# Kernel tuning notes

Measured on AMD Instinct MI355X. Metric: run time of the kernel, lower is better.

The kernel has to match this reference:

```python
import jax, jax.numpy as jnp
import numpy as np

N_NODES = 100000
N_EDGES = 1000000
LATENT = 128
EMBED = 32


def setup_inputs() -> dict:
    key = jax.random.key(0)
    ks = jax.random.split(key, 10)
    z = jax.random.normal(ks[0], (N_NODES, LATENT), dtype=jnp.float32)
    edge_index = jax.random.randint(ks[1], (2, N_EDGES), 0, N_NODES, dtype=jnp.int64)
    bond_types = jax.random.randint(ks[2], (N_EDGES,), 0, 13, dtype=jnp.int64)
    d_in = 2 * LATENT + EMBED  # 288
    s = lambda k, shape, fan: jax.random.normal(k, shape, dtype=jnp.float32) / np.sqrt(fan)
    embed = s(ks[3], (13, EMBED), EMBED)
    W1 = s(ks[4], (d_in, LATENT), d_in)
    b1 = jnp.zeros((LATENT,), jnp.float32)
    W2 = s(ks[5], (LATENT, 64), LATENT)
    b2 = jnp.zeros((64,), jnp.float32)
    W3 = s(ks[6], (64, 1), 64)
    b3 = jnp.zeros((1,), jnp.float32)
    return {"z": z, "edge_index": edge_index, "bond_types": bond_types,
            "embed": embed, "W1": W1, "b1": b1, "W2": W2, "b2": b2,
            "W3": W3, "b3": b3}


def reference(z, edge_index, bond_types, embed, W1, b1, W2, b2, W3, b3):
    src, dst = edge_index[0], edge_index[1]
    # gather endpoint latents and bond-type embedding, concat -> [E, 288]
    features = jnp.concatenate([z[src], z[dst], embed[bond_types]], axis=-1)
    h = jax.nn.relu(features @ W1 + b1)   # dropout is identity in eval mode
    h = jax.nn.relu(h @ W2 + b2)
    out = jax.nn.softplus(h @ W3 + b3)
    return out.squeeze(-1)  # [E]
```

## Files before the change

### kernel.cpp

```cpp
#include <hip/hip_runtime.h>

#define E_EDGES 1000000
#define BM 64
#define NBLK (E_EDGES / BM)
#define DIN 288
#define PADA 296
#define H1DIM 128
#define PAD1 136
#define H2DIM 64
#define PAD2 68
#define NNODES 100000
#define LATENT 128

#define WT1_OFF 0
#define WT2_OFF (DIN * H1DIM)
#define EMB_OFF (WT2_OFF + H1DIM * H2DIM)
#define ZB_OFF  46080
#define WS_NEED ((size_t)(ZB_OFF + NNODES * LATENT) * 2)

typedef __bf16 v8bf __attribute__((ext_vector_type(8)));
typedef __bf16 v4bf __attribute__((ext_vector_type(4)));
typedef float  v4f  __attribute__((ext_vector_type(4)));

__device__ __forceinline__ void cvt_store4(__bf16* p, float4 v) {
    v4bf o;
    o[0] = (__bf16)v.x; o[1] = (__bf16)v.y; o[2] = (__bf16)v.z; o[3] = (__bf16)v.w;
    *(v4bf*)p = o;
}

__global__ void prep_kernel(const float* __restrict__ W1, const float* __restrict__ W2,
                            const float* __restrict__ z, const float* __restrict__ embed,
                            __bf16* __restrict__ ws, int do_z) {
    int i = blockIdx.x * 256 + threadIdx.x;
    if (do_z) {
        int i4 = i * 4;
        if (i4 < NNODES * LATENT) {
            float4 v = *(const float4*)(z + i4);
            cvt_store4(ws + ZB_OFF + i4, v);
        }
    }
    if (i < DIN * H1DIM) {
        int n = i / DIN, k = i - n * DIN;
        ws[WT1_OFF + i] = (__bf16)W1[k * H1DIM + n];
    }
    if (i < H1DIM * H2DIM) {
        int n = i / H1DIM, k = i - n * H1DIM;
        ws[WT2_OFF + i] = (__bf16)W2[k * H2DIM + n];
    }
    if (i < 13 * 32) ws[EMB_OFF + i] = (__bf16)embed[i];
}

template <bool ZBF16>
__global__ __launch_bounds__(256, 4) void fused_kernel(
    const float* __restrict__ z, const int* __restrict__ eidx,
    const int* __restrict__ bt, const float* __restrict__ embed,
    const float* __restrict__ b1, const float* __restrict__ b2,
    const float* __restrict__ W3, const float* __restrict__ b3,
    const __bf16* __restrict__ ws, float* __restrict__ out)
{
    __shared__ __bf16 sA[BM * PADA];
    __shared__ float sb1[H1DIM];
    __shared__ float sb2[H2DIM];
    __shared__ float sw3[H2DIM];
    __shared__ float sb3;
    __bf16* sH1 = sA;
    __bf16* sH2 = sA + BM * PAD1;

    const __bf16* wt1  = ws + WT1_OFF;
    const __bf16* wt2  = ws + WT2_OFF;
    const __bf16* embb = ws + EMB_OFF;
    const __bf16* zb   = ws + ZB_OFF;

    const int tid = threadIdx.x;
    const int e0 = blockIdx.x * BM;

    if (tid < 128) {
        sb1[tid] = b1[tid];
    } else if (tid < 192) {
        sb2[tid - 128] = b2[tid - 128];
    } else {
        int k = tid - 192;
        sw3[k] = W3[k];
        if (k == 0) sb3 = b3[0];
    }

    {
        const int r = tid >> 2;
        const int j = tid & 3;
        const int e = e0 + r;
        const int isrc = eidx[e];
        const int idst = eidx[E_EDGES + e];
        const int ib   = bt[e];
        __bf16* rowp = &sA[r * PADA];
        if constexpr (ZBF16) {
            const v8bf* zs = (const v8bf*)(zb + (size_t)isrc * LATENT);
            const v8bf* zd = (const v8bf*)(zb + (size_t)idst * LATENT);
            const v8bf* em = (const v8bf*)(embb + ib * 32);
            #pragma unroll
            for (int i = 0; i < 4; ++i) {
                int p = i * 4 + j;
                *(v8bf*)(rowp + p * 8) = zs[p];
            }
            #pragma unroll
            for (int i = 0; i < 4; ++i) {
                int p = i * 4 + j;
                *(v8bf*)(rowp + 128 + p * 8) = zd[p];
            }
            *(v8bf*)(rowp + 256 + j * 8) = em[j];
        } else {
            const float4* zs = (const float4*)(z + (size_t)isrc * LATENT);
            const float4* zd = (const float4*)(z + (size_t)idst * LATENT);
            const float4* em = (const float4*)(embed + (size_t)ib * 32);
            #pragma unroll
            for (int i = 0; i < 8; ++i) { int p = i * 4 + j; cvt_store4(rowp + p * 4, zs[p]); }
            #pragma unroll
            for (int i = 0; i < 8; ++i) { int p = i * 4 + j; cvt_store4(rowp + 128 + p * 4, zd[p]); }
            #pragma unroll
            for (int i = 0; i < 2; ++i) { int p = i * 4 + j; cvt_store4(rowp + 256 + p * 4, em[p]); }
        }
    }
    __syncthreads();

    const int wave  = tid >> 6;
    const int lane  = tid & 63;
    const int quad  = lane >> 4;
    const int col16 = lane & 15;

    v4f zero4 = {0.f, 0.f, 0.f, 0.f};
    v4f acc[4][2];
    #pragma unroll
    for (int mt = 0; mt < 4; ++mt) { acc[mt][0] = zero4; acc[mt][1] = zero4; }

    const __bf16* w1p0 = wt1 + (size_t)(wave * 32 + col16) * DIN;
    const __bf16* w1p1 = wt1 + (size_t)(wave * 32 + 16 + col16) * DIN;

    #pragma unroll
    for (int ks = 0; ks < 9; ++ks) {
        int k0 = ks * 32 + quad * 8;
        v8bf a0 = *(const v8bf*)&sA[(0 * 16 + col16) * PADA + k0];
        v8bf a1 = *(const v8bf*)&sA[(1 * 16 + col16) * PADA + k0];
        v8bf a2 = *(const v8bf*)&sA[(2 * 16 + col16) * PADA + k0];
        v8bf a3 = *(const v8bf*)&sA[(3 * 16 + col16) * PADA + k0];
        v8bf bb0 = *(const v8bf*)&w1p0[k0];
        v8bf bb1 = *(const v8bf*)&w1p1[k0];
        acc[0][0] = __builtin_amdgcn_mfma_f32_16x16x32_bf16(a0, bb0, acc[0][0], 0, 0, 0);
        acc[1][0] = __builtin_amdgcn_mfma_f32_16x16x32_bf16(a1, bb0, acc[1][0], 0, 0, 0);
        acc[2][0] = __builtin_amdgcn_mfma_f32_16x16x32_bf16(a2, bb0, acc[2][0], 0, 0, 0);
        acc[3][0] = __builtin_amdgcn_mfma_f32_16x16x32_bf16(a3, bb0, acc[3][0], 0, 0, 0);
        acc[0][1] = __builtin_amdgcn_mfma_f32_16x16x32_bf16(a0, bb1, acc[0][1], 0, 0, 0);
        acc[1][1] = __builtin_amdgcn_mfma_f32_16x16x32_bf16(a1, bb1, acc[1][1], 0, 0, 0);
        acc[2][1] = __builtin_amdgcn_mfma_f32_16x16x32_bf16(a2, bb1, acc[2][1], 0, 0, 0);
        acc[3][1] = __builtin_amdgcn_mfma_f32_16x16x32_bf16(a3, bb1, acc[3][1], 0, 0, 0);
    }
    __syncthreads();

    #pragma unroll
    for (int j = 0; j < 2; ++j) {
        int n = wave * 32 + j * 16 + col16;
        float bias = sb1[n];
        #pragma unroll
        for (int mt = 0; mt < 4; ++mt) {
            #pragma unroll
            for (int r = 0; r < 4; ++r) {
                int m = mt * 16 + quad * 4 + r;
                float h = acc[mt][j][r] + bias;
                sH1[m * PAD1 + n] = (__bf16)fmaxf(h, 0.f);
            }
        }
    }
    __syncthreads();

    v4f acc2[4];
    #pragma unroll
    for (int mt = 0; mt < 4; ++mt) acc2[mt] = zero4;

    const __bf16* w2p = wt2 + (size_t)(wave * 16 + col16) * H1DIM;
    #pragma unroll
    for (int ks = 0; ks < 4; ++ks) {
        int k0 = ks * 32 + quad * 8;
        v8bf bb = *(const v8bf*)&w2p[k0];
        #pragma unroll
        for (int mt = 0; mt < 4; ++mt) {
            v8bf aa = *(const v8bf*)&sH1[(mt * 16 + col16) * PAD1 + k0];
            acc2[mt] = __builtin_amdgcn_mfma_f32_16x16x32_bf16(aa, bb, acc2[mt], 0, 0, 0);
        }
    }
    {
        int n = wave * 16 + col16;
        float bias = sb2[n];
        #pragma unroll
        for (int mt = 0; mt < 4; ++mt) {
            #pragma unroll
            for (int r = 0; r < 4; ++r) {
                int m = mt * 16 + quad * 4 + r;
                sH2[m * PAD2 + n] = (__bf16)fmaxf(acc2[mt][r] + bias, 0.f);
            }
        }
    }
    __syncthreads();

    {
        int row = tid >> 2;
        int q   = tid & 3;
        float s = 0.f;
        #pragma unroll
        for (int kk = 0; kk < 16; ++kk) {
            int k = q * 16 + kk;
            s += (float)sH2[row * PAD2 + k] * sw3[k];
        }
        s += __shfl_xor(s, 1);
        s += __shfl_xor(s, 2);
        if (q == 0) {
            float x = s + sb3;
            float sp = fmaxf(x, 0.f) + log1pf(expf(-fabsf(x)));
            out[e0 + row] = sp;
        }
    }
}

extern "C" void kernel_launch(void* const* d_in, const int* in_sizes, int n_in,
                              void* d_out, int out_size, void* d_ws, size_t ws_size,
                              hipStream_t stream) {
    const float* z     = (const float*)d_in[0];
    const int*   eidx  = (const int*)d_in[1];
    const int*   btyp  = (const int*)d_in[2];
    const float* embed = (const float*)d_in[3];
    const float* W1    = (const float*)d_in[4];
    const float* b1    = (const float*)d_in[5];
    const float* W2    = (const float*)d_in[6];
    const float* b2    = (const float*)d_in[7];
    const float* W3    = (const float*)d_in[8];
    const float* b3    = (const float*)d_in[9];
    float* out = (float*)d_out;
    __bf16* ws = (__bf16*)d_ws;

    bool big_ws = (ws_size >= WS_NEED);
    if (big_ws) {
        int n4 = (NNODES * LATENT / 4 + 255) / 256;
        prep_kernel<<<n4, 256, 0, stream>>>(W1, W2, z, embed, ws, 1);
        fused_kernel<true><<<NBLK, 256, 0, stream>>>(z, eidx, btyp, embed,
                                                     b1, b2, W3, b3, ws, out);
    } else {
        prep_kernel<<<(DIN * H1DIM + 255) / 256, 256, 0, stream>>>(W1, W2, z, embed, ws, 0);
        fused_kernel<false><<<NBLK, 256, 0, stream>>>(z, eidx, btyp, embed,
                                                      b1, b2, W3, b3, ws, out);
    }
}
```

Before: 244.2 us.

## Retile MLP waves to 2x2 grid and fuse layer-3 dot into layer-2 registers

```diff
diff --git a/kernel.cpp b/kernel.cpp
--- a/kernel.cpp
+++ b/kernel.cpp
@@ -7,14 +7,12 @@
 #define PADA 296
 #define H1DIM 128
 #define PAD1 136
-#define H2DIM 64
-#define PAD2 68
 #define NNODES 100000
 #define LATENT 128
 
 #define WT1_OFF 0
 #define WT2_OFF (DIN * H1DIM)
-#define EMB_OFF (WT2_OFF + H1DIM * H2DIM)
+#define EMB_OFF (WT2_OFF + H1DIM * 64)
 #define ZB_OFF  46080
 #define WS_NEED ((size_t)(ZB_OFF + NNODES * LATENT) * 2)
 
@@ -43,9 +41,9 @@
         int n = i / DIN, k = i - n * DIN;
         ws[WT1_OFF + i] = (__bf16)W1[k * H1DIM + n];
     }
-    if (i < H1DIM * H2DIM) {
+    if (i < H1DIM * 64) {
         int n = i / H1DIM, k = i - n * H1DIM;
-        ws[WT2_OFF + i] = (__bf16)W2[k * H2DIM + n];
+        ws[WT2_OFF + i] = (__bf16)W2[k * 64 + n];
     }
     if (i < 13 * 32) ws[EMB_OFF + i] = (__bf16)embed[i];
 }
@@ -60,11 +58,10 @@
 {
     __shared__ __bf16 sA[BM * PADA];
     __shared__ float sb1[H1DIM];
-    __shared__ float sb2[H2DIM];
-    __shared__ float sw3[H2DIM];
-    __shared__ float sb3;
+    __shared__ float sb2[64];
+    __shared__ float sw3[64];
+    __shared__ float sb3s;
     __bf16* sH1 = sA;
-    __bf16* sH2 = sA + BM * PAD1;
 
     const __bf16* wt1  = ws + WT1_OFF;
     const __bf16* wt2  = ws + WT2_OFF;
@@ -81,7 +78,7 @@
     } else {
         int k = tid - 192;
         sw3[k] = W3[k];
-        if (k == 0) sb3 = b3[0];
+        if (k == 0) sb3s = b3[0];
     }
 
     {
@@ -97,15 +94,9 @@
             const v8bf* zd = (const v8bf*)(zb + (size_t)idst * LATENT);
             const v8bf* em = (const v8bf*)(embb + ib * 32);
             #pragma unroll
-            for (int i = 0; i < 4; ++i) {
-                int p = i * 4 + j;
-                *(v8bf*)(rowp + p * 8) = zs[p];
-            }
-            #pragma unroll
-            for (int i = 0; i < 4; ++i) {
-                int p = i * 4 + j;
-                *(v8bf*)(rowp + 128 + p * 8) = zd[p];
-            }
+            for (int i = 0; i < 4; ++i) { int p = i * 4 + j; *(v8bf*)(rowp + p * 8) = zs[p]; }
+            #pragma unroll
+            for (int i = 0; i < 4; ++i) { int p = i * 4 + j; *(v8bf*)(rowp + 128 + p * 8) = zd[p]; }
             *(v8bf*)(rowp + 256 + j * 8) = em[j];
         } else {
             const float4* zs = (const float4*)(z + (size_t)isrc * LATENT);
@@ -125,46 +116,56 @@
     const int lane  = tid & 63;
     const int quad  = lane >> 4;
     const int col16 = lane & 15;
+    const int wm = wave >> 1;
+    const int wn = wave & 1;
 
     v4f zero4 = {0.f, 0.f, 0.f, 0.f};
-    v4f acc[4][2];
-    #pragma unroll
-    for (int mt = 0; mt < 4; ++mt) { acc[mt][0] = zero4; acc[mt][1] = zero4; }
-
-    const __bf16* w1p0 = wt1 + (size_t)(wave * 32 + col16) * DIN;
-    const __bf16* w1p1 = wt1 + (size_t)(wave * 32 + 16 + col16) * DIN;
+    v4f acc[2][4];
+    #pragma unroll
+    for (int mt = 0; mt < 2; ++mt)
+        #pragma unroll
+        for (int jj = 0; jj < 4; ++jj) acc[mt][jj] = zero4;
+
+    const __bf16* w1p0 = wt1 + (size_t)(wn * 64 + 4 * col16 + 0) * DIN;
+    const __bf16* w1p1 = wt1 + (size_t)(wn * 64 + 4 * col16 + 1) * DIN;
+    const __bf16* w1p2 = wt1 + (size_t)(wn * 64 + 4 * col16 + 2) * DIN;
+    const __bf16* w1p3 = wt1 + (size_t)(wn * 64 + 4 * col16 + 3) * DIN;
+    const int arow0 = (wm * 32 + col16) * PADA;
+    const int arow1 = (wm * 32 + 16 + col16) * PADA;
 
     #pragma unroll
     for (int ks = 0; ks < 9; ++ks) {
         int k0 = ks * 32 + quad * 8;
-        v8bf a0 = *(const v8bf*)&sA[(0 * 16 + col16) * PADA + k0];
-        v8bf a1 = *(const v8bf*)&sA[(1 * 16 + col16) * PADA + k0];
-        v8bf a2 = *(const v8bf*)&sA[(2 * 16 + col16) * PADA + k0];
-        v8bf a3 = *(const v8bf*)&sA[(3 * 16 + col16) * PADA + k0];
+        v8bf a0 = *(const v8bf*)&sA[arow0 + k0];
+        v8bf a1 = *(const v8bf*)&sA[arow1 + k0];
         v8bf bb0 = *(const v8bf*)&w1p0[k0];
         v8bf bb1 = *(const v8bf*)&w1p1[k0];
+        v8bf bb2 = *(const v8bf*)&w1p2[k0];
+        v8bf bb3 = *(const v8bf*)&w1p3[k0];
         acc[0][0] = __builtin_amdgcn_mfma_f32_16x16x32_bf16(a0, bb0, acc[0][0], 0, 0, 0);
         acc[1][0] = __builtin_amdgcn_mfma_f32_16x16x32_bf16(a1, bb0, acc[1][0], 0, 0, 0);
-        acc[2][0] = __builtin_amdgcn_mfma_f32_16x16x32_bf16(a2, bb0, acc[2][0], 0, 0, 0);
-        acc[3][0] = __builtin_amdgcn_mfma_f32_16x16x32_bf16(a3, bb0, acc[3][0], 0, 0, 0);
         acc[0][1] = __builtin_amdgcn_mfma_f32_16x16x32_bf16(a0, bb1, acc[0][1], 0, 0, 0);
         acc[1][1] = __builtin_amdgcn_mfma_f32_16x16x32_bf16(a1, bb1, acc[1][1], 0, 0, 0);
-        acc[2][1] = __builtin_amdgcn_mfma_f32_16x16x32_bf16(a2, bb1, acc[2][1], 0, 0, 0);
-        acc[3][1] = __builtin_amdgcn_mfma_f32_16x16x32_bf16(a3, bb1, acc[3][1], 0, 0, 0);
+        acc[0][2] = __builtin_amdgcn_mfma_f32_16x16x32_bf16(a0, bb2, acc[0][2], 0, 0, 0);
+        acc[1][2] = __builtin_amdgcn_mfma_f32_16x16x32_bf16(a1, bb2, acc[1][2], 0, 0, 0);
+        acc[0][3] = __builtin_amdgcn_mfma_f32_16x16x32_bf16(a0, bb3, acc[0][3], 0, 0, 0);
+        acc[1][3] = __builtin_amdgcn_mfma_f32_16x16x32_bf16(a1, bb3, acc[1][3], 0, 0, 0);
     }
     __syncthreads();
 
-    #pragma unroll
-    for (int j = 0; j < 2; ++j) {
-        int n = wave * 32 + j * 16 + col16;
-        float bias = sb1[n];
-        #pragma unroll
-        for (int mt = 0; mt < 4; ++mt) {
+    {
+        float4 bias1 = *(const float4*)&sb1[wn * 64 + 4 * col16];
+        #pragma unroll
+        for (int mt = 0; mt < 2; ++mt) {
             #pragma unroll
             for (int r = 0; r < 4; ++r) {
-                int m = mt * 16 + quad * 4 + r;
-                float h = acc[mt][j][r] + bias;
-                sH1[m * PAD1 + n] = (__bf16)fmaxf(h, 0.f);
+                v4bf o;
+                o[0] = (__bf16)fmaxf(acc[mt][0][r] + bias1.x, 0.f);
+                o[1] = (__bf16)fmaxf(acc[mt][1][r] + bias1.y, 0.f);
+                o[2] = (__bf16)fmaxf(acc[mt][2][r] + bias1.z, 0.f);
+                o[3] = (__bf16)fmaxf(acc[mt][3][r] + bias1.w, 0.f);
+                int m = wm * 32 + mt * 16 + quad * 4 + r;
+                *(v4bf*)&sH1[m * PAD1 + wn * 64 + 4 * col16] = o;
             }
         }
     }
@@ -172,48 +173,42 @@
 
     v4f acc2[4];
     #pragma unroll
-    for (int mt = 0; mt < 4; ++mt) acc2[mt] = zero4;
-
-    const __bf16* w2p = wt2 + (size_t)(wave * 16 + col16) * H1DIM;
+    for (int nt = 0; nt < 4; ++nt) acc2[nt] = zero4;
+
+    const int hrow = (wave * 16 + col16) * PAD1;
     #pragma unroll
     for (int ks = 0; ks < 4; ++ks) {
         int k0 = ks * 32 + quad * 8;
-        v8bf bb = *(const v8bf*)&w2p[k0];
-        #pragma unroll
-        for (int mt = 0; mt < 4; ++mt) {
-            v8bf aa = *(const v8bf*)&sH1[(mt * 16 + col16) * PAD1 + k0];
-            acc2[mt] = __builtin_amdgcn_mfma_f32_16x16x32_bf16(aa, bb, acc2[mt], 0, 0, 0);
-        }
-    }
+        v8bf aa = *(const v8bf*)&sH1[hrow + k0];
+        #pragma unroll
+        for (int nt = 0; nt < 4; ++nt) {
+            v8bf bb = *(const v8bf*)&wt2[(size_t)(nt * 16 + col16) * H1DIM + k0];
+            acc2[nt] = __builtin_amdgcn_mfma_f32_16x16x32_bf16(aa, bb, acc2[nt], 0, 0, 0);
+        }
+    }
+
     {
-        int n = wave * 16 + col16;
-        float bias = sb2[n];
-        #pragma unroll
-        for (int mt = 0; mt < 4; ++mt) {
-            #pragma unroll
-            for (int r = 0; r < 4; ++r) {
-                int m = mt * 16 + quad * 4 + r;
-                sH2[m * PAD2 + n] = (__bf16)fmaxf(acc2[mt][r] + bias, 0.f);
+        float b2v[4], w3v[4];
+        #pragma unroll
+        for (int nt = 0; nt < 4; ++nt) {
+            b2v[nt] = sb2[nt * 16 + col16];
+            w3v[nt] = sw3[nt * 16 + col16];
+        }
+        float b3v = sb3s;
+        #pragma unroll
+        for (int r = 0; r < 4; ++r) {
+            float s = 0.f;
+            #pragma unroll
+            for (int nt = 0; nt < 4; ++nt)
+                s += fmaxf(acc2[nt][r] + b2v[nt], 0.f) * w3v[nt];
+            s += __shfl_xor(s, 1);
+            s += __shfl_xor(s, 2);
+            s += __shfl_xor(s, 4);
+            s += __shfl_xor(s, 8);
+            if (col16 == 0) {
+                float x = s + b3v;
+                out[e0 + wave * 16 + quad * 4 + r] = fmaxf(x, 0.f) + log1pf(expf(-fabsf(x)));
             }
-        }
-    }
-    __syncthreads();
-
-    {
-        int row = tid >> 2;
-        int q   = tid & 3;
-        float s = 0.f;
-        #pragma unroll
-        for (int kk = 0; kk < 16; ++kk) {
-            int k = q * 16 + kk;
-            s += (float)sH2[row * PAD2 + k] * sw3[k];
-        }
-        s += __shfl_xor(s, 1);
-        s += __shfl_xor(s, 2);
-        if (q == 0) {
-            float x = s + sb3;
-            float sp = fmaxf(x, 0.f) + log1pf(expf(-fabsf(x)));
-            out[e0 + row] = sp;
         }
     }
 }
```

Measured after the change: 483.8 us. 1.98x slower.

## Transpose layer-2 MFMA so each wave owns edges and fuse layer 3 in registers

Applied to the files above, without the earlier changes.

```diff
diff --git a/kernel.cpp b/kernel.cpp
--- a/kernel.cpp
+++ b/kernel.cpp
@@ -7,14 +7,12 @@
 #define PADA 296
 #define H1DIM 128
 #define PAD1 136
-#define H2DIM 64
-#define PAD2 68
 #define NNODES 100000
 #define LATENT 128
 
 #define WT1_OFF 0
 #define WT2_OFF (DIN * H1DIM)
-#define EMB_OFF (WT2_OFF + H1DIM * H2DIM)
+#define EMB_OFF (WT2_OFF + H1DIM * 64)
 #define ZB_OFF  46080
 #define WS_NEED ((size_t)(ZB_OFF + NNODES * LATENT) * 2)
 
@@ -43,9 +41,9 @@
         int n = i / DIN, k = i - n * DIN;
         ws[WT1_OFF + i] = (__bf16)W1[k * H1DIM + n];
     }
-    if (i < H1DIM * H2DIM) {
+    if (i < H1DIM * 64) {
         int n = i / H1DIM, k = i - n * H1DIM;
-        ws[WT2_OFF + i] = (__bf16)W2[k * H2DIM + n];
+        ws[WT2_OFF + i] = (__bf16)W2[k * 64 + n];
     }
     if (i < 13 * 32) ws[EMB_OFF + i] = (__bf16)embed[i];
 }
@@ -60,11 +58,10 @@
 {
     __shared__ __bf16 sA[BM * PADA];
     __shared__ float sb1[H1DIM];
-    __shared__ float sb2[H2DIM];
-    __shared__ float sw3[H2DIM];
-    __shared__ float sb3;
+    __shared__ float sb2[64];
+    __shared__ float sw3[64];
+    __shared__ float sb3s;
     __bf16* sH1 = sA;
-    __bf16* sH2 = sA + BM * PAD1;
 
     const __bf16* wt1  = ws + WT1_OFF;
     const __bf16* wt2  = ws + WT2_OFF;
@@ -81,7 +78,7 @@
     } else {
         int k = tid - 192;
         sw3[k] = W3[k];
-        if (k == 0) sb3 = b3[0];
+        if (k == 0) sb3s = b3[0];
     }
 
     {
@@ -97,15 +94,9 @@
             const v8bf* zd = (const v8bf*)(zb + (size_t)idst * LATENT);
             const v8bf* em = (const v8bf*)(embb + ib * 32);
             #pragma unroll
-            for (int i = 0; i < 4; ++i) {
-                int p = i * 4 + j;
-                *(v8bf*)(rowp + p * 8) = zs[p];
-            }
-            #pragma unroll
-            for (int i = 0; i < 4; ++i) {
-                int p = i * 4 + j;
-                *(v8bf*)(rowp + 128 + p * 8) = zd[p];
-            }
+            for (int i = 0; i < 4; ++i) { int p = i * 4 + j; *(v8bf*)(rowp + p * 8) = zs[p]; }
+            #pragma unroll
+            for (int i = 0; i < 4; ++i) { int p = i * 4 + j; *(v8bf*)(rowp + 128 + p * 8) = zd[p]; }
             *(v8bf*)(rowp + 256 + j * 8) = em[j];
         } else {
             const float4* zs = (const float4*)(z + (size_t)isrc * LATENT);
@@ -172,48 +163,35 @@
 
     v4f acc2[4];
     #pragma unroll
-    for (int mt = 0; mt < 4; ++mt) acc2[mt] = zero4;
-
-    const __bf16* w2p = wt2 + (size_t)(wave * 16 + col16) * H1DIM;
+    for (int nt = 0; nt < 4; ++nt) acc2[nt] = zero4;
+
+    const int hrow = (wave * 16 + col16) * PAD1;
     #pragma unroll
     for (int ks = 0; ks < 4; ++ks) {
         int k0 = ks * 32 + quad * 8;
-        v8bf bb = *(const v8bf*)&w2p[k0];
+        v8bf bfrag = *(const v8bf*)&sH1[hrow + k0];
         #pragma unroll
-        for (int mt = 0; mt < 4; ++mt) {
-            v8bf aa = *(const v8bf*)&sH1[(mt * 16 + col16) * PAD1 + k0];
-            acc2[mt] = __builtin_amdgcn_mfma_f32_16x16x32_bf16(aa, bb, acc2[mt], 0, 0, 0);
-        }
-    }
+        for (int nt = 0; nt < 4; ++nt) {
+            v8bf afrag = *(const v8bf*)&wt2[(size_t)(nt * 16 + col16) * H1DIM + k0];
+            acc2[nt] = __builtin_amdgcn_mfma_f32_16x16x32_bf16(afrag, bfrag, acc2[nt], 0, 0, 0);
+        }
+    }
+
     {
-        int n = wave * 16 + col16;
-        float bias = sb2[n];
-        #pragma unroll
-        for (int mt = 0; mt < 4; ++mt) {
-            #pragma unroll
-            for (int r = 0; r < 4; ++r) {
-                int m = mt * 16 + quad * 4 + r;
-                sH2[m * PAD2 + n] = (__bf16)fmaxf(acc2[mt][r] + bias, 0.f);
-            }
-        }
-    }
-    __syncthreads();
-
-    {
-        int row = tid >> 2;
-        int q   = tid & 3;
         float s = 0.f;
         #pragma unroll
-        for (int kk = 0; kk < 16; ++kk) {
-            int k = q * 16 + kk;
-            s += (float)sH2[row * PAD2 + k] * sw3[k];
-        }
-        s += __shfl_xor(s, 1);
-        s += __shfl_xor(s, 2);
-        if (q == 0) {
-            float x = s + sb3;
-            float sp = fmaxf(x, 0.f) + log1pf(expf(-fabsf(x)));
-            out[e0 + row] = sp;
+        for (int nt = 0; nt < 4; ++nt) {
+            #pragma unroll
+            for (int r = 0; r < 4; ++r) {
+                int f = nt * 16 + quad * 4 + r;
+                s += fmaxf(acc2[nt][r] + sb2[f], 0.f) * sw3[f];
+            }
+        }
+        s += __shfl_xor(s, 16);
+        s += __shfl_xor(s, 32);
+        if (quad == 0) {
+            float x = s + sb3s;
+            out[e0 + wave * 16 + col16] = fmaxf(x, 0.f) + log1pf(expf(-fabsf(x)));
         }
     }
 }
```

New measurement: 316.1 us. 29.5% more time.
